# Optimization experiments

Hardware: AMD Instinct MI355X
Metric: run time of the kernel (lower is better)

## Reference

```python
import jax, jax.numpy as jnp
import numpy as np

POOL = (2, 2)  # pool_size from init


def setup_inputs() -> dict:
    key = jax.random.key(0)
    k1, k2 = jax.random.split(key)
    B, H, W, C = 8, 128, 128, 256
    Ho, Wo = H * POOL[0], W * POOL[1]
    inputs = jax.random.normal(k1, (B, H, W, C), dtype=jnp.float32)
    # argmax-style indices: per-batch offsets into flattened (Ho, Wo, C)
    indices = jax.random.randint(k2, (B, H, W, C), 0, Ho * Wo * C, dtype=jnp.int32)
    return {"inputs": inputs, "indices": indices}


def reference(inputs, indices):
    # Faithful to MaxUnpooling2D.call: scatter pooled values into a
    # zero-initialized tensor of shape (B, H*ph, W*pw, C) at argmax positions.
    B, H, W, C = inputs.shape
    Ho, Wo = H * POOL[0], W * POOL[1]
    flat_out = Ho * Wo * C  # per-batch flat output size
    # add per-batch offset (mirrors batch_range * flat_output_shape[1])
    batch_off = (jnp.arange(B, dtype=indices.dtype) * flat_out)[:, None]
    flat_idx = indices.reshape(B, -1) + batch_off  # [B, H*W*C]
    out = jnp.zeros((B * flat_out,), dtype=inputs.dtype)
    # tf.scatter_nd sums duplicate indices -> .at[].add matches
    out = out.at[flat_idx.reshape(-1)].add(inputs.reshape(-1))
    return out.reshape(B, Ho, Wo, C)
```

## Files before the change

### kernel.cpp

```cpp
#include <hip/hip_runtime.h>
#include <stdint.h>


#define LOG2_REGION 14
#define REGION      (1 << LOG2_REGION)
#define NB          (1 << (24 - LOG2_REGION))
#define NBUCKETS    (8 * NB)
#define SUB         16384
#define BLOCK1      1024
#define GRID1       ((1 << 25) / SUB)
#define PADM        3
#define BLOCK2      512

__global__ __launch_bounds__(BLOCK1) void bin_pairs(
    const int*   __restrict__ idx,
    const float* __restrict__ val,
    int*         __restrict__ counters,
    uint64_t*    __restrict__ pairs,
    int cap)
{
    __shared__ uint64_t stage[SUB];
    __shared__ int hist[NB];
    __shared__ int pos[NB];
    __shared__ int delta[NB];
    __shared__ int wsumI[16];

    const int tid  = threadIdx.x;
    const int lane = tid & 63;
    const int wave = tid >> 6;
    const long long start = (long long)blockIdx.x * SUB;
    const int batch = (int)(start >> 22);
    const int4*   idx4 = (const int4*)(idx + start);
    const float4* val4 = (const float4*)(val + start);

    hist[tid] = 0;
    __syncthreads();

    int4 iv[4];
    #pragma unroll
    for (int it = 0; it < 4; ++it) {
        iv[it] = idx4[it * BLOCK1 + tid];
        atomicAdd(&hist[iv[it].x >> LOG2_REGION], 1);
        atomicAdd(&hist[iv[it].y >> LOG2_REGION], 1);
        atomicAdd(&hist[iv[it].z >> LOG2_REGION], 1);
        atomicAdd(&hist[iv[it].w >> LOG2_REGION], 1);
    }
    __syncthreads();

    const int h  = hist[tid];
    const int hp = (h + PADM) & ~PADM;
    int v = h;
    #pragma unroll
    for (int d = 1; d < 64; d <<= 1) {
        int u = __shfl_up(v, d);
        if (lane >= d) v += u;
    }
    if (lane == 63) wsumI[wave] = v;
    __syncthreads();
    if (tid < 16) {
        int t = wsumI[tid];
        #pragma unroll
        for (int d = 1; d < 16; d <<= 1) {
            int u = __shfl_up(t, d);
            if (tid >= d) t += u;
        }
        wsumI[tid] = t;
    }
    __syncthreads();
    const int lstart = v + (wave ? wsumI[wave - 1] : 0) - h;
    pos[tid] = lstart;
    int gbase = 0;
    if (hp) gbase = atomicAdd(&counters[batch * NB + tid], hp);
    delta[tid] = gbase - lstart;

    uint64_t* pb = pairs + (uint64_t)batch * NB * (uint64_t)cap;

    {
        const uint64_t padp = (uint64_t)(uint32_t)(tid << LOG2_REGION);
        for (int j = h; j < hp; ++j) {
            int dst = gbase + j;
            if (dst < cap) pb[(uint64_t)tid * cap + dst] = padp;
        }
    }
    __syncthreads();

    #pragma unroll
    for (int it = 0; it < 4; ++it) {
        float4 vv = val4[it * BLOCK1 + tid];
        int   ia[4] = {iv[it].x, iv[it].y, iv[it].z, iv[it].w};
        float fa[4] = {vv.x, vv.y, vv.z, vv.w};
        #pragma unroll
        for (int k = 0; k < 4; ++k) {
            int b = ia[k] >> LOG2_REGION;
            int l = atomicAdd(&pos[b], 1);
            stage[l] = (uint64_t)(uint32_t)ia[k]
                     | ((uint64_t)__float_as_uint(fa[k]) << 32);
        }
    }
    __syncthreads();

    for (int i = tid; i < SUB; i += BLOCK1) {
        uint64_t p = stage[i];
        int b = (int)((uint32_t)p >> LOG2_REGION);
        int dst = i + delta[b];
        if (dst < cap)
            pb[(uint64_t)b * cap + dst] = p;
    }
}

__global__ __launch_bounds__(BLOCK2) void accumulate(
    const uint64_t* __restrict__ pairs,
    const int*      __restrict__ counters,
    float*          __restrict__ out,
    int cap)
{
    __shared__ float acc[REGION];
    const int b = blockIdx.x;
    const int tid = threadIdx.x;

    float4* acc4 = (float4*)acc;
    #pragma unroll
    for (int i = tid; i < REGION / 4; i += BLOCK2)
        acc4[i] = make_float4(0.f, 0.f, 0.f, 0.f);
    __syncthreads();

    int n = counters[b];
    if (n > cap) n = cap;
    const ulonglong2* p2 = (const ulonglong2*)(pairs + (uint64_t)b * cap);
    for (int i = tid; i < (n >> 1); i += BLOCK2) {
        ulonglong2 v = p2[i];
        atomicAdd(&acc[(int)(v.x & (REGION - 1))],
                  __uint_as_float((uint32_t)(v.x >> 32)));
        atomicAdd(&acc[(int)(v.y & (REGION - 1))],
                  __uint_as_float((uint32_t)(v.y >> 32)));
    }
    __syncthreads();

    float4* o4 = (float4*)(out + ((long long)b << LOG2_REGION));
    #pragma unroll
    for (int i = tid; i < REGION / 4; i += BLOCK2)
        o4[i] = acc4[i];
}

extern "C" void kernel_launch(void* const* d_in, const int* in_sizes, int n_in,
                              void* d_out, int out_size, void* d_ws, size_t ws_size,
                              hipStream_t stream) {
    const float* in  = (const float*)d_in[0];
    const int*   idx = (const int*)d_in[1];
    float*       out = (float*)d_out;

    int*      counters = (int*)d_ws;
    uint64_t* pairs    = (uint64_t*)((char*)d_ws + 65536);

    int cap = (int)(((ws_size - 65536) / 8) / NBUCKETS);
    if (cap > 8192) cap = 8192;
    cap &= ~PADM;

    hipMemsetAsync(counters, 0, NBUCKETS * sizeof(int), stream);
    bin_pairs<<<GRID1, BLOCK1, 0, stream>>>(idx, in, counters, pairs, cap);
    accumulate<<<NBUCKETS, BLOCK2, 0, stream>>>(pairs, counters, out, cap);
}
```

Before: 958.6 us.

## Double accumulation region size and stage bucket padding in shared memory

Raises the per-bucket output region from 16K to 32K floats, which halves the number of buckets. The accumulate kernel now uses 1024 threads and 128KB of LDS per block, and bucket capacity is raised to match. In the binning kernel, the padding entries are now written into the shared staging buffer at the end of each bucket, so they go out with the coalesced flush instead of as scattered global stores. The larger LDS footprint lowers occupancy in accumulate but gives fewer, longer bucket segments.

```diff
diff --git a/kernel.cpp b/kernel.cpp
--- a/kernel.cpp
+++ b/kernel.cpp
@@ -2,7 +2,7 @@
 #include <stdint.h>
 
 
-#define LOG2_REGION 14
+#define LOG2_REGION 15
 #define REGION      (1 << LOG2_REGION)
 #define NB          (1 << (24 - LOG2_REGION))
 #define NBUCKETS    (8 * NB)
@@ -10,7 +10,8 @@
 #define BLOCK1      1024
 #define GRID1       ((1 << 25) / SUB)
 #define PADM        3
-#define BLOCK2      512
+#define STAGE_CAP   (SUB + PADM * NB)
+#define BLOCK2      1024
 
 __global__ __launch_bounds__(BLOCK1) void bin_pairs(
     const int*   __restrict__ idx,
@@ -19,7 +20,7 @@
     uint64_t*    __restrict__ pairs,
     int cap)
 {
-    __shared__ uint64_t stage[SUB];
+    __shared__ uint64_t stage[STAGE_CAP];
     __shared__ int hist[NB];
     __shared__ int pos[NB];
     __shared__ int delta[NB];
@@ -33,12 +34,13 @@
     const int4*   idx4 = (const int4*)(idx + start);
     const float4* val4 = (const float4*)(val + start);
 
-    hist[tid] = 0;
+    if (tid < NB) hist[tid] = 0;
     __syncthreads();
 
-    int4 iv[4];
+    const int ITER = SUB / 4 / BLOCK1;
+    int4 iv[ITER];
     #pragma unroll
-    for (int it = 0; it < 4; ++it) {
+    for (int it = 0; it < ITER; ++it) {
         iv[it] = idx4[it * BLOCK1 + tid];
         atomicAdd(&hist[iv[it].x >> LOG2_REGION], 1);
         atomicAdd(&hist[iv[it].y >> LOG2_REGION], 1);
@@ -47,9 +49,9 @@
     }
     __syncthreads();
 
-    const int h  = hist[tid];
-    const int hp = (h + PADM) & ~PADM;
-    int v = h;
+    int h = 0, hp = 0;
+    if (tid < NB) { h = hist[tid]; hp = (h + PADM) & ~PADM; }
+    int v = hp;
     #pragma unroll
     for (int d = 1; d < 64; d <<= 1) {
         int u = __shfl_up(v, d);
@@ -57,35 +59,27 @@
     }
     if (lane == 63) wsumI[wave] = v;
     __syncthreads();
-    if (tid < 16) {
+    if (tid < 8) {
         int t = wsumI[tid];
         #pragma unroll
-        for (int d = 1; d < 16; d <<= 1) {
+        for (int d = 1; d < 8; d <<= 1) {
             int u = __shfl_up(t, d);
             if (tid >= d) t += u;
         }
         wsumI[tid] = t;
     }
     __syncthreads();
-    const int lstart = v + (wave ? wsumI[wave - 1] : 0) - h;
-    pos[tid] = lstart;
+    const int lstart = v + (wave ? wsumI[wave - 1] : 0) - hp;
     int gbase = 0;
-    if (hp) gbase = atomicAdd(&counters[batch * NB + tid], hp);
-    delta[tid] = gbase - lstart;
-
-    uint64_t* pb = pairs + (uint64_t)batch * NB * (uint64_t)cap;
-
-    {
-        const uint64_t padp = (uint64_t)(uint32_t)(tid << LOG2_REGION);
-        for (int j = h; j < hp; ++j) {
-            int dst = gbase + j;
-            if (dst < cap) pb[(uint64_t)tid * cap + dst] = padp;
-        }
+    if (tid < NB) {
+        pos[tid] = lstart;
+        if (hp) gbase = atomicAdd(&counters[batch * NB + tid], hp);
+        delta[tid] = gbase - lstart;
     }
     __syncthreads();
 
     #pragma unroll
-    for (int it = 0; it < 4; ++it) {
+    for (int it = 0; it < ITER; ++it) {
         float4 vv = val4[it * BLOCK1 + tid];
         int   ia[4] = {iv[it].x, iv[it].y, iv[it].z, iv[it].w};
         float fa[4] = {vv.x, vv.y, vv.z, vv.w};
@@ -99,7 +93,17 @@
     }
     __syncthreads();
 
-    for (int i = tid; i < SUB; i += BLOCK1) {
+    if (tid < NB) {
+        const uint64_t padp = (uint64_t)(uint32_t)(tid << LOG2_REGION);
+        #pragma unroll
+        for (int j = 0; j < PADM; ++j)
+            if (h + j < hp) stage[lstart + h + j] = padp;
+    }
+    __syncthreads();
+
+    const int total = wsumI[7];
+    uint64_t* pb = pairs + (uint64_t)batch * NB * (uint64_t)cap;
+    for (int i = tid; i < total; i += BLOCK1) {
         uint64_t p = stage[i];
         int b = (int)((uint32_t)p >> LOG2_REGION);
         int dst = i + delta[b];
@@ -153,7 +157,7 @@
     uint64_t* pairs    = (uint64_t*)((char*)d_ws + 65536);
 
     int cap = (int)(((ws_size - 65536) / 8) / NBUCKETS);
-    if (cap > 8192) cap = 8192;
+    if (cap > 16384) cap = 16384;
     cap &= ~PADM;
 
     hipMemsetAsync(counters, 0, NBUCKETS * sizeof(int), stream);
```

New measurement: 907.1 us. -5.4%, faster.
